# Optimization experiments

Hardware: AMD Instinct MI355X
Metric: run time of the kernel (lower is better)

The kernel has to match this reference:

```python
import jax, jax.numpy as jnp
import numpy as np
from jax import lax

HEAD_DIM = 32
SCALE = HEAD_DIM ** -0.5
BN_EPS = 1e-5


def _bn_relu(x, g, b):
    # training-mode BatchNorm2d over (B,H,W) per channel, biased variance, then ReLU
    mean = jnp.mean(x, axis=(0, 1, 2))
    var = jnp.var(x, axis=(0, 1, 2))
    y = (x - mean) * lax.rsqrt(var + BN_EPS) * g + b
    return jax.nn.relu(y)


def _pool2x2(y, op):
    # AvgPool2d/MaxPool2d(kernel=2, stride=2) on [B,pH,pW,C]
    B, pH, pW, C = y.shape
    y = y.reshape(B, pH // 2, 2, pW // 2, 2, C)
    return op(y, axis=(2, 4))


def setup_inputs() -> dict:
    key = jax.random.key(0)
    ks = jax.random.split(key, 12)
    B, H, W, C, pC = 16, 32, 32, 512, 256
    s = lambda k, shape, fan: jax.random.normal(k, shape, jnp.float32) * (fan ** -0.5)
    return {
        "x": jax.random.normal(ks[0], (B, H, W, C), jnp.float32),
        "prevx": jax.random.normal(ks[1], (B, 2 * H, 2 * W, pC), jnp.float32),
        "w_prev_qkv": s(ks[2], (C, pC), pC),          # Linear(prev_dim->dim), no bias
        "w_qkv": s(ks[3], (C, C), C),                  # Linear(dim->dim), no bias
        "fuse_w": s(ks[4], (2 * C, C), 2 * C),         # 1x1 conv as [Cin, Cout]
        "fuse_b": jax.random.normal(ks[5], (C,), jnp.float32) * 0.01,
        "bn1_g": jnp.ones((C,), jnp.float32) + jax.random.normal(ks[6], (C,), jnp.float32) * 0.01,
        "bn1_b": jax.random.normal(ks[7], (C,), jnp.float32) * 0.01,
        "out_w": s(ks[8], (3, 3, C, C), 9 * C),        # 3x3 conv HWIO
        "out_b": jax.random.normal(ks[9], (C,), jnp.float32) * 0.01,
        "bn2_g": jnp.ones((C,), jnp.float32) + jax.random.normal(ks[10], (C,), jnp.float32) * 0.01,
        "bn2_b": jax.random.normal(ks[11], (C,), jnp.float32) * 0.01,
        "gamma": jnp.array([0.3], jnp.float32),
        "beta": jnp.array([0.4], jnp.float32),
    }


def reference(x, prevx, w_prev_qkv, w_qkv, fuse_w, fuse_b, bn1_g, bn1_b,
              out_w, out_b, bn2_g, bn2_b, gamma, beta):
    B, H, W, C = x.shape
    N = H * W

    prevqkv = prevx @ w_prev_qkv.T                       # [B,2H,2W,C]
    qkv = (x @ w_qkv.T).reshape(B, N, C)                 # [B,N,C]
    avg_kv = _pool2x2(prevqkv, jnp.mean).reshape(B, -1, C)
    max_kv = _pool2x2(prevqkv, jnp.max).reshape(B, -1, C)

    def attn(q, k, v):
        a = jax.nn.softmax(jnp.einsum('bnc,bmc->bnm', q, k) * SCALE, axis=-1)
        o = jnp.einsum('bnm,bmc->bnc', a, v)
        # faithful to torch: (attn@v).transpose(1,2).reshape(B,H,W,-1)
        return jnp.swapaxes(o, 1, 2).reshape(B, H, W, C)

    x_now = attn(qkv, qkv, qkv)
    avgx_prev = attn(qkv, avg_kv, avg_kv)
    maxx_prev = attn(qkv, max_kv, max_kv)
    x_prev = beta[0] * avgx_prev + (1.0 - beta[0]) * maxx_prev

    cat = jnp.concatenate([x_now, x_prev], axis=-1)      # [B,H,W,2C]
    fusx = _bn_relu(jnp.einsum('bhwi,io->bhwo', cat, fuse_w) + fuse_b, bn1_g, bn1_b)
    x = x + gamma[0] * fusx

    y = lax.conv_general_dilated(x, out_w, window_strides=(1, 1), padding='SAME',
                                 dimension_numbers=('NHWC', 'HWIO', 'NHWC')) + out_b
    return _bn_relu(y, bn2_g, bn2_b)
```

## Files before the change

kernel.cpp:

```cpp
#include <hip/hip_runtime.h>
#include <hip/hip_bf16.h>

#define B_   16
#define C_   512
#define N_   1024
#define NTOK 16384
#define SCALE_ 0.17677669529663687f
#define EPS_ 1e-5f

typedef __attribute__((ext_vector_type(8))) short bf16x8;
typedef __attribute__((ext_vector_type(4))) float f32x4;
typedef __attribute__((ext_vector_type(4))) short sh4;

#define GLOBAL_AS __attribute__((address_space(1)))
#define LDS_AS    __attribute__((address_space(3)))
#define MFMA16 __builtin_amdgcn_mfma_f32_16x16x32_bf16

__device__ __forceinline__ short f2bs(float v){
    __hip_bfloat16 h = __float2bfloat16(v);
    return *reinterpret_cast<short*>(&h);
}
__device__ __forceinline__ float bs2f(short s){
    __hip_bfloat16 h = *reinterpret_cast<__hip_bfloat16*>(&s);
    return __bfloat162float(h);
}
__device__ __forceinline__ void gload16(const void* g, void* l){
    __builtin_amdgcn_global_load_lds((const GLOBAL_AS unsigned int*)g,
                                     (LDS_AS unsigned int*)l, 16, 0, 0);
}

enum { AG_ROW = 0, AG_POOL = 1, AG_FUSE = 2, AG_CONV = 3, AG_SEL3 = 4 };
enum { EP_QKV = 0, EP_POOL = 1, EP_BIAS_F32 = 5, EP_SPLIT_F32 = 6, EP_PVN = 7 };
enum { ORD_INNER_N = 0, ORD_INNER_M = 1 };

__global__ __launch_bounds__(256) void k_zero(float* p, int n){
    int i = blockIdx.x*256 + threadIdx.x;
    if (i < n) p[i] = 0.f;
}

__global__ __launch_bounds__(256) void k_cast(const float* __restrict__ s, short* __restrict__ d, int n){
    int i = (blockIdx.x*256 + threadIdx.x)*4;
    if (i >= n) return;
    float4 v = *reinterpret_cast<const float4*>(s + i);
    sh4 o; o[0]=f2bs(v.x); o[1]=f2bs(v.y); o[2]=f2bs(v.z); o[3]=f2bs(v.w);
    *reinterpret_cast<sh4*>(d + i) = o;
}

__global__ __launch_bounds__(256) void k_tcast(const float* __restrict__ src, short* __restrict__ dst,
                                               int R, int Cc){
    __shared__ float t[32][33];
    int bx = blockIdx.x*32, by = blockIdx.y*32;
    int tx = threadIdx.x & 31, ty = threadIdx.x >> 5;
    #pragma unroll
    for (int i = 0; i < 32; i += 8)
        t[ty+i][tx] = src[(size_t)(by+ty+i)*Cc + bx+tx];
    __syncthreads();
    #pragma unroll
    for (int i = 0; i < 32; i += 8)
        dst[(size_t)(bx+ty+i)*R + by+tx] = f2bs(t[tx][ty+i]);
}

template<int AM, int EP, int ORDER, int NX, int NY, int NZ, int NT, int KT, int KROW, int KSPLIT,
         long ASTR, long BSTR>
__global__ __launch_bounds__(256) void k_mm(const short* __restrict__ A,
                                            const short* __restrict__ Bt,
                                            const short* __restrict__ A2,
                                            const float* __restrict__ sc0,
                                            void* __restrict__ O0,
                                            void* __restrict__ O1,
                                            void* __restrict__ O2,
                                            void* __restrict__ O3){
    __shared__ short Asm[128*32];
    __shared__ short Bsm[128*32];
    const int tid = threadIdx.x, wave = tid >> 6, lane = tid & 63;

    constexpr int nwg = NX*NY*NZ;
    constexpr int q8 = nwg >> 3, r8 = nwg & 7;
    int orig = blockIdx.x;
    int xcd = orig & 7, idx8 = orig >> 3;
    int wg = (xcd < r8 ? xcd*(q8+1) : r8*(q8+1) + (xcd - r8)*q8) + idx8;
    int bz = wg / (NX*NY);
    int rem = wg - bz*(NX*NY);
    int nx, my;
    if constexpr (ORDER == ORD_INNER_N){ my = rem / NX; nx = rem - my*NX; }
    else                               { nx = rem / NY; my = rem - nx*NY; }

    const int m0 = my*128, n0 = nx*128;
    const short* Ab;
    if constexpr (AM == AG_SEL3){
        const short* base = (bz < 16) ? A : (bz < 32) ? A2 : (const short*)O3;
        Ab = base + (size_t)(bz & 15)*ASTR;
    } else {
        Ab = A + (size_t)bz*ASTR;
    }
    const short* Bb = Bt + (size_t)bz*BSTR;

    f32x4 acc[4][4];
    #pragma unroll
    for (int i = 0; i < 4; ++i)
        #pragma unroll
        for (int j = 0; j < 4; ++j)
            acc[i][j] = (f32x4){0.f,0.f,0.f,0.f};

    const int wm = (wave >> 1)*64, wn = (wave & 1)*64;
    const int lrow = lane & 15, lk = (lane >> 4)*8;

    for (int k0 = 0; k0 < KT; k0 += 32){
        #pragma unroll
        for (int is = 0; is < 2; ++is){
            int fl = is*256 + tid;
            int r = fl >> 2, ccol = (fl & 3)*8;
            int kk = bz*KSPLIT + k0 + ccol;
            const short* ga;
            if constexpr (AM == AG_ROW || AM == AG_SEL3){
                ga = Ab + (size_t)(m0 + r)*KROW + kk;
            } else if constexpr (AM == AG_POOL){
                int m = m0 + r;
                int b = m >> 12, rem2 = m & 4095, g = rem2 >> 2, qd = rem2 & 3;
                int srow = (b*64 + (g>>5)*2 + (qd>>1))*64 + (g&31)*2 + (qd&1);
                ga = Ab + (size_t)srow*KROW + kk;
            } else if constexpr (AM == AG_FUSE){
                int m = m0 + r;
                int b = m >> 10, rem2 = m & 1023, h = rem2 >> 5, w = rem2 & 31;
                const short* src = (kk < 512) ? A : A2;
                ga = src + ((size_t)(b*512 + h*16 + (w>>1))*1024 + ((w&1)<<9) + (kk & 511));
            } else {
                int m = m0 + r;
                int b = m >> 10, rem2 = m & 1023, h = rem2 >> 5, w = rem2 & 31;
                int tap = kk >> 9, ic = kk & 511;
                int dh = tap/3 - 1, dw = tap - (tap/3)*3 - 1;
                int hs = h + dh, wd = w + dw;
                if (hs >= 0 && hs < 32 && wd >= 0 && wd < 32)
                    ga = A + ((size_t)((b*32 + hs)*32 + wd)*512 + ic);
                else
                    ga = A2;
            }
            gload16(ga, &Asm[(is*4 + wave)*512]);
            const short* gb = Bb + (size_t)(n0 + r)*KROW + kk;
            gload16(gb, &Bsm[(is*4 + wave)*512]);
        }
        __syncthreads();
        bf16x8 af[4], bfr[4];
        #pragma unroll
        for (int mi = 0; mi < 4; ++mi)
            af[mi] = *(const bf16x8*)&Asm[(wm + mi*16 + lrow)*32 + lk];
        #pragma unroll
        for (int nj = 0; nj < 4; ++nj)
            bfr[nj] = *(const bf16x8*)&Bsm[(wn + nj*16 + lrow)*32 + lk];
        #pragma unroll
        for (int mi = 0; mi < 4; ++mi)
            #pragma unroll
            for (int nj = 0; nj < 4; ++nj)
                acc[mi][nj] = MFMA16(af[mi], bfr[nj], acc[mi][nj], 0, 0, 0);
        __syncthreads();
    }

    const int lg = lane >> 4;
    #pragma unroll
    for (int mi = 0; mi < 4; ++mi)
        #pragma unroll
        for (int nj = 0; nj < 4; ++nj){
            int c  = n0 + wn + nj*16 + lrow;
            int r0 = m0 + wm + mi*16 + lg*4;
            f32x4 v = acc[mi][nj];
            if constexpr (EP == EP_QKV){
                sh4 t4;
                #pragma unroll
                for (int rg = 0; rg < 4; ++rg){
                    short s = f2bs(v[rg]);
                    ((short*)O0)[(size_t)(r0+rg)*NT + c] = s;
                    t4[rg] = s;
                }
                int b = r0 >> 10, t = r0 & 1023;
                *reinterpret_cast<sh4*>((short*)O1 + ((size_t)(b*512 + c))*1024 + t) = t4;
            } else if constexpr (EP == EP_POOL){
                float av = 0.25f*(v[0]+v[1]+v[2]+v[3]);
                float mx = fmaxf(fmaxf(v[0],v[1]), fmaxf(v[2],v[3]));
                int g = r0 >> 2;
                int b = g >> 10, t = g & 1023;
                ((short*)O0)[(size_t)g*512 + c] = f2bs(av);
                ((short*)O2)[(size_t)g*512 + c] = f2bs(mx);
                ((short*)O1)[((size_t)(b*512 + c))*1024 + t] = f2bs(av);
                ((short*)O3)[((size_t)(b*512 + c))*1024 + t] = f2bs(mx);
            } else if constexpr (EP == EP_PVN){
                short* Ob = ((bz < 16) ? (short*)O0 : (bz < 32) ? (short*)O1 : (short*)O2)
                            + (size_t)(bz & 15)*524288;
                float sc = sc0[(size_t)bz*1024 + c];
                #pragma unroll
                for (int rg = 0; rg < 4; ++rg)
                    Ob[(size_t)(r0+rg)*NT + c] = f2bs(v[rg]*sc);
            } else if constexpr (EP == EP_SPLIT_F32){
                float* O = (float*)O0 + (size_t)bz*((long)NTOK*NT);
                #pragma unroll
                for (int rg = 0; rg < 4; ++rg)
                    O[(size_t)(r0+rg)*NT + c] = v[rg];
            } else {
                float bias = sc0[c];
                #pragma unroll
                for (int rg = 0; rg < 4; ++rg)
                    ((float*)O0)[(size_t)(r0+rg)*NT + c] = v[rg] + bias;
            }
        }
}

__global__ __launch_bounds__(256) void k_scorep(
    const short* __restrict__ Q,
    const short* __restrict__ K0, const short* __restrict__ K1, const short* __restrict__ K2,
    short* __restrict__ P, float* __restrict__ linvp)
{
    __shared__ short Kls[32*512];
    __shared__ short Pls[4][16][40];

    const int tid = threadIdx.x, wave = tid >> 6, lane = tid & 63;
    const int lrow = lane & 15, hi = lane >> 4;

    int orig = blockIdx.x;
    int wg = (orig & 7)*96 + (orig >> 3);
    int a = wg >> 8, rem = wg & 255;
    int b = rem >> 4, qt = rem & 15;

    const short* Kb = (a == 0 ? K0 : a == 1 ? K1 : K2) + (size_t)b*524288;
    const short* Qb = Q + (size_t)b*524288;
    short* Pb = P + ((size_t)(a*16 + b) << 20);
    const int m0 = qt*64 + wave*16;

    bf16x8 q[16];
    #pragma unroll
    for (int ks = 0; ks < 16; ++ks)
        q[ks] = *(const bf16x8*)&Qb[(size_t)(m0 + lrow)*512 + ks*32 + hi*8];

    const int swk = (lrow & 7) << 4;
    float lsum[4] = {0.f,0.f,0.f,0.f};

    for (int kv = 0; kv < 1024; kv += 32){
        #pragma unroll
        for (int it = 0; it < 8; ++it){
            int r = it*4 + wave;
            gload16(Kb + (size_t)(kv + r)*512 + (size_t)((lane ^ (r & 7))*8), &Kls[r*512]);
        }
        __syncthreads();
        f32x4 s0 = {0.f,0.f,0.f,0.f}, s1 = {0.f,0.f,0.f,0.f};
        #pragma unroll
        for (int ks = 0; ks < 16; ++ks){
            bf16x8 b0 = *(const bf16x8*)&Kls[lrow*512      + (((ks*64 + hi*16) ^ swk) >> 1)];
            bf16x8 b1 = *(const bf16x8*)&Kls[(16+lrow)*512 + (((ks*64 + hi*16) ^ swk) >> 1)];
            s0 = MFMA16(q[ks], b0, s0, 0, 0, 0);
            s1 = MFMA16(q[ks], b1, s1, 0, 0, 0);
        }
        #pragma unroll
        for (int r = 0; r < 4; ++r){
            float p0 = __expf(fminf(s0[r]*SCALE_, 80.f));
            float p1 = __expf(fminf(s1[r]*SCALE_, 80.f));
            lsum[r] += p0 + p1;
            Pls[wave][hi*4 + r][lrow]      = f2bs(p0);
            Pls[wave][hi*4 + r][16 + lrow] = f2bs(p1);
        }
        bf16x8 pk = *(const bf16x8*)&Pls[wave][lane >> 2][(lane & 3)*8];
        *reinterpret_cast<bf16x8*>(&Pb[(size_t)(m0 + (lane >> 2))*1024 + kv + (lane & 3)*8]) = pk;
        __syncthreads();
    }

    #pragma unroll
    for (int r = 0; r < 4; ++r){
        float s = lsum[r];
        #pragma unroll
        for (int off = 1; off < 16; off <<= 1) s += __shfl_xor(s, off);
        if (lrow == 0)
            linvp[(size_t)(a*16 + b)*1024 + m0 + hi*4 + r] = 1.f/s;
    }
}

__global__ __launch_bounds__(256) void k_combine(const short* __restrict__ av,
                                                 const short* __restrict__ mx,
                                                 short* __restrict__ o,
                                                 const float* __restrict__ beta){
    int i = (blockIdx.x*256 + threadIdx.x)*8;
    float be = beta[0];
    bf16x8 va = *(const bf16x8*)&av[i];
    bf16x8 vm = *(const bf16x8*)&mx[i];
    bf16x8 vo;
    #pragma unroll
    for (int j = 0; j < 8; ++j)
        vo[j] = f2bs(be*bs2f(va[j]) + (1.f - be)*bs2f(vm[j]));
    *reinterpret_cast<bf16x8*>(&o[i]) = vo;
}

__global__ __launch_bounds__(256) void k_stats(const float* __restrict__ in,
                                               float* __restrict__ sum, float* __restrict__ sumsq){
    int t = threadIdx.x, c0 = t*2, r0 = blockIdx.x*32;
    float s0=0, s1=0, q0=0, q1=0;
    for (int r = 0; r < 32; ++r){
        float2 v = *reinterpret_cast<const float2*>(in + (size_t)(r0+r)*C_ + c0);
        s0 += v.x; q0 += v.x*v.x; s1 += v.y; q1 += v.y*v.y;
    }
    atomicAdd(&sum[c0],   s0); atomicAdd(&sum[c0+1],   s1);
    atomicAdd(&sumsq[c0], q0); atomicAdd(&sumsq[c0+1], q1);
}

__global__ __launch_bounds__(256) void k_stats2(const float* __restrict__ p0,
                                                const float* __restrict__ p1,
                                                const float* __restrict__ bias,
                                                float* __restrict__ Y,
                                                float* __restrict__ sum, float* __restrict__ sumsq){
    int t = threadIdx.x, c0 = t*2, r0 = blockIdx.x*32;
    float b0 = bias[c0], b1 = bias[c0+1];
    float s0=0, s1=0, q0=0, q1=0;
    for (int r = 0; r < 32; ++r){
        size_t off = (size_t)(r0+r)*C_ + c0;
        float2 a = *reinterpret_cast<const float2*>(p0 + off);
        float2 b = *reinterpret_cast<const float2*>(p1 + off);
        float v0 = a.x + b.x + b0, v1 = a.y + b.y + b1;
        float2 ov; ov.x = v0; ov.y = v1;
        *reinterpret_cast<float2*>(Y + off) = ov;
        s0 += v0; q0 += v0*v0; s1 += v1; q1 += v1*v1;
    }
    atomicAdd(&sum[c0],   s0); atomicAdd(&sum[c0+1],   s1);
    atomicAdd(&sumsq[c0], q0); atomicAdd(&sumsq[c0+1], q1);
}

__global__ __launch_bounds__(256) void k_apply1(const float* __restrict__ fusx,
                                                const float* __restrict__ x,
                                                const float* __restrict__ sum,
                                                const float* __restrict__ sumsq,
                                                const float* __restrict__ g,
                                                const float* __restrict__ bb,
                                                const float* __restrict__ gamma,
                                                short* __restrict__ x2q){
    int idx = blockIdx.x*256 + threadIdx.x;
    int c = idx & (C_-1);
    float mean = sum[c]*(1.f/NTOK);
    float var  = sumsq[c]*(1.f/NTOK) - mean*mean;
    float t = (fusx[idx] - mean)*rsqrtf(var + EPS_)*g[c] + bb[c];
    x2q[idx] = f2bs(x[idx] + gamma[0]*fmaxf(t, 0.f));
}

__global__ __launch_bounds__(256) void k_apply2(float* __restrict__ Y,
                                                const float* __restrict__ sum,
                                                const float* __restrict__ sumsq,
                                                const float* __restrict__ g,
                                                const float* __restrict__ bb){
    int idx = blockIdx.x*256 + threadIdx.x;
    int c = idx & (C_-1);
    float mean = sum[c]*(1.f/NTOK);
    float var  = sumsq[c]*(1.f/NTOK) - mean*mean;
    float t = (Y[idx] - mean)*rsqrtf(var + EPS_)*g[c] + bb[c];
    Y[idx] = fmaxf(t, 0.f);
}

extern "C" void kernel_launch(void* const* d_in, const int* in_sizes, int n_in,
                              void* d_out, int out_size, void* d_ws, size_t ws_size,
                              hipStream_t stream){
    const float* x      = (const float*)d_in[0];
    const float* prevx  = (const float*)d_in[1];
    const float* w_prev = (const float*)d_in[2];
    const float* w_qkv  = (const float*)d_in[3];
    const float* fuse_w = (const float*)d_in[4];
    const float* fuse_b = (const float*)d_in[5];
    const float* bn1_g  = (const float*)d_in[6];
    const float* bn1_b  = (const float*)d_in[7];
    const float* out_w  = (const float*)d_in[8];
    const float* out_b  = (const float*)d_in[9];
    const float* bn2_g  = (const float*)d_in[10];
    const float* bn2_b  = (const float*)d_in[11];
    const float* gamma  = (const float*)d_in[12];
    const float* beta   = (const float*)d_in[13];
    float* out = (float*)d_out;

    char* ws8 = (char*)d_ws;
    short* pxq  = (short*)(ws8 + 0);
    short* xq   = (short*)(ws8 + 33554432);
    short* Pall = (short*)(ws8 + 0);
    float* cpart= (float*)(ws8 + 0);
    short* qkvT = (short*)(ws8 + 100663296);
    short* x2q  = (short*)(ws8 + 100663296);
    short* avgkT= (short*)(ws8 + 117440512);
    short* maxkT= (short*)(ws8 + 134217728);
    short* prevT= maxkT;
    short* nowT = (short*)(ws8 + 150994944);
    short* avgk = nowT;
    short* avgT = (short*)(ws8 + 167772160);
    short* maxk = avgT;
    short* maxT = (short*)(ws8 + 184549376);
    float* fusx = (float*)(ws8 + 184549376);
    short* qkv  = (short*)(ws8 + 201326592);
    short* wqT  = (short*)(ws8 + 218103808);
    short* wpT  = (short*)(ws8 + 218628096);
    short* wfT  = (short*)(ws8 + 218890240);
    short* wcT  = (short*)(ws8 + 219938816);
    float* st   = (float*)(ws8 + 224657408);
    short* zpg  = (short*)(ws8 + 224665600);
    float* linv = (float*)(ws8 + 224666624);
    float *s1sum = st, *s1sq = st + 512, *s2sum = st + 1024, *s2sq = st + 1536;

    dim3 blk(256);
    k_zero<<<9, blk, 0, stream>>>(st, 2304);
    k_cast<<<8192, blk, 0, stream>>>(x, xq, 8388608);
    k_cast<<<256,  blk, 0, stream>>>(w_qkv, wqT, 262144);
    k_cast<<<128,  blk, 0, stream>>>(w_prev, wpT, 131072);
    k_tcast<<<dim3(16, 32),  blk, 0, stream>>>(fuse_w, wfT, 1024, 512);
    k_tcast<<<dim3(16, 144), blk, 0, stream>>>(out_w, wcT, 4608, 512);
    k_cast<<<16384, blk, 0, stream>>>(prevx, pxq, 16777216);

    k_mm<AG_ROW, EP_QKV, ORD_INNER_N, 4, 128, 1, 512, 512, 512, 0, 0L, 0L>
        <<<512, blk, 0, stream>>>(xq, wqT, nullptr, nullptr,
                                  qkv, qkvT, nullptr, nullptr);
    k_mm<AG_POOL, EP_POOL, ORD_INNER_N, 4, 512, 1, 512, 256, 256, 0, 0L, 0L>
        <<<2048, blk, 0, stream>>>(pxq, wpT, nullptr, nullptr,
                                   avgk, avgkT, maxk, maxkT);
    k_scorep<<<768, blk, 0, stream>>>(qkv, qkv, avgk, maxk, Pall, linv);
    k_mm<AG_SEL3, EP_PVN, ORD_INNER_M, 8, 4, 48, 1024, 1024, 1024, 0, 524288L, 1048576L>
        <<<1536, blk, 0, stream>>>(qkvT, Pall, avgkT, linv,
                                   nowT, avgT, maxT, maxkT);
    k_combine<<<4096, blk, 0, stream>>>(avgT, maxT, prevT, beta);
    k_mm<AG_FUSE, EP_BIAS_F32, ORD_INNER_N, 4, 128, 1, 512, 1024, 1024, 0, 0L, 0L>
        <<<512, blk, 0, stream>>>(nowT, wfT, prevT, fuse_b,
                                  fusx, nullptr, nullptr, nullptr);
    k_stats<<<512, blk, 0, stream>>>(fusx, s1sum, s1sq);
    k_apply1<<<32768, blk, 0, stream>>>(fusx, x, s1sum, s1sq, bn1_g, bn1_b, gamma, x2q);
    k_mm<AG_CONV, EP_SPLIT_F32, ORD_INNER_N, 4, 128, 2, 512, 2304, 4608, 2304, 0L, 0L>
        <<<1024, blk, 0, stream>>>(x2q, wcT, zpg, nullptr,
                                   cpart, nullptr, nullptr, nullptr);
    k_stats2<<<512, blk, 0, stream>>>(cpart, cpart + (size_t)NTOK*C_, out_b, out, s2sum, s2sq);
    k_apply2<<<32768, blk, 0, stream>>>(out, s2sum, s2sq, bn2_g, bn2_b);
}
```

Baseline: 518.3 us.

## Fuse BN1 statistics into fuse GEMM epilogue and store intermediates as bf16

```diff
diff --git a/kernel.cpp b/kernel.cpp
--- a/kernel.cpp
+++ b/kernel.cpp
@@ -30,7 +30,7 @@
 }
 
 enum { AG_ROW = 0, AG_POOL = 1, AG_FUSE = 2, AG_CONV = 3, AG_SEL3 = 4 };
-enum { EP_QKV = 0, EP_POOL = 1, EP_BIAS_F32 = 5, EP_SPLIT_F32 = 6, EP_PVN = 7 };
+enum { EP_QKV = 0, EP_POOL = 1, EP_PVN = 7, EP_FUSE_STATS = 8, EP_SPLIT_BF16 = 9 };
 enum { ORD_INNER_N = 0, ORD_INNER_M = 1 };
 
 __global__ __launch_bounds__(256) void k_zero(float* p, int n){
@@ -156,6 +156,41 @@
     }
 
     const int lg = lane >> 4;
+
+    if constexpr (EP == EP_FUSE_STATS){
+        float* redS = (float*)Asm;
+        float* redQ = (float*)Bsm;
+        #pragma unroll
+        for (int nj = 0; nj < 4; ++nj){
+            int c = n0 + wn + nj*16 + lrow;
+            float bias = sc0[c];
+            float s = 0.f, qq = 0.f;
+            #pragma unroll
+            for (int mi = 0; mi < 4; ++mi){
+                int r0 = m0 + wm + mi*16 + lg*4;
+                #pragma unroll
+                for (int rg = 0; rg < 4; ++rg){
+                    float val = acc[mi][nj][rg] + bias;
+                    s += val; qq += val*val;
+                    ((short*)O0)[(size_t)(r0+rg)*NT + c] = f2bs(val);
+                }
+            }
+            int chl = wn + nj*16 + lrow;
+            int slot = (wave >> 1)*4 + lg;
+            redS[chl*8 + slot] = s;
+            redQ[chl*8 + slot] = qq;
+        }
+        __syncthreads();
+        if (tid < 128){
+            float S = 0.f, Q = 0.f;
+            #pragma unroll
+            for (int k = 0; k < 8; ++k){ S += redS[tid*8 + k]; Q += redQ[tid*8 + k]; }
+            atomicAdd(&((float*)O1)[n0 + tid], S);
+            atomicAdd(&((float*)O2)[n0 + tid], Q);
+        }
+        return;
+    }
+
     #pragma unroll
     for (int mi = 0; mi < 4; ++mi)
         #pragma unroll
@@ -189,16 +224,11 @@
                 #pragma unroll
                 for (int rg = 0; rg < 4; ++rg)
                     Ob[(size_t)(r0+rg)*NT + c] = f2bs(v[rg]*sc);
-            } else if constexpr (EP == EP_SPLIT_F32){
-                float* O = (float*)O0 + (size_t)bz*((long)NTOK*NT);
+            } else {
+                short* O = (short*)O0 + (size_t)bz*((long)NTOK*NT);
                 #pragma unroll
                 for (int rg = 0; rg < 4; ++rg)
-                    O[(size_t)(r0+rg)*NT + c] = v[rg];
-            } else {
-                float bias = sc0[c];
-                #pragma unroll
-                for (int rg = 0; rg < 4; ++rg)
-                    ((float*)O0)[(size_t)(r0+rg)*NT + c] = v[rg] + bias;
+                    O[(size_t)(r0+rg)*NT + c] = f2bs(v[rg]);
             }
         }
 }
@@ -285,20 +315,8 @@
     *reinterpret_cast<bf16x8*>(&o[i]) = vo;
 }
 
-__global__ __launch_bounds__(256) void k_stats(const float* __restrict__ in,
-                                               float* __restrict__ sum, float* __restrict__ sumsq){
-    int t = threadIdx.x, c0 = t*2, r0 = blockIdx.x*32;
-    float s0=0, s1=0, q0=0, q1=0;
-    for (int r = 0; r < 32; ++r){
-        float2 v = *reinterpret_cast<const float2*>(in + (size_t)(r0+r)*C_ + c0);
-        s0 += v.x; q0 += v.x*v.x; s1 += v.y; q1 += v.y*v.y;
-    }
-    atomicAdd(&sum[c0],   s0); atomicAdd(&sum[c0+1],   s1);
-    atomicAdd(&sumsq[c0], q0); atomicAdd(&sumsq[c0+1], q1);
-}
-
-__global__ __launch_bounds__(256) void k_stats2(const float* __restrict__ p0,
-                                                const float* __restrict__ p1,
+__global__ __launch_bounds__(256) void k_stats2(const short* __restrict__ p0,
+                                                const short* __restrict__ p1,
                                                 const float* __restrict__ bias,
                                                 float* __restrict__ Y,
                                                 float* __restrict__ sum, float* __restrict__ sumsq){
@@ -307,9 +325,10 @@
     float s0=0, s1=0, q0=0, q1=0;
     for (int r = 0; r < 32; ++r){
         size_t off = (size_t)(r0+r)*C_ + c0;
-        float2 a = *reinterpret_cast<const float2*>(p0 + off);
-        float2 b = *reinterpret_cast<const float2*>(p1 + off);
-        float v0 = a.x + b.x + b0, v1 = a.y + b.y + b1;
+        unsigned a = *reinterpret_cast<const unsigned*>(p0 + off);
+        unsigned b = *reinterpret_cast<const unsigned*>(p1 + off);
+        float v0 = bs2f((short)(a & 0xffff)) + bs2f((short)(b & 0xffff)) + b0;
+        float v1 = bs2f((short)(a >> 16))    + bs2f((short)(b >> 16))    + b1;
         float2 ov; ov.x = v0; ov.y = v1;
         *reinterpret_cast<float2*>(Y + off) = ov;
         s0 += v0; q0 += v0*v0; s1 += v1; q1 += v1*v1;
@@ -318,7 +337,7 @@
     atomicAdd(&sumsq[c0], q0); atomicAdd(&sumsq[c0+1], q1);
 }
 
-__global__ __launch_bounds__(256) void k_apply1(const float* __restrict__ fusx,
+__global__ __launch_bounds__(256) void k_apply1(const short* __restrict__ fusxq,
                                                 const float* __restrict__ x,
                                                 const float* __restrict__ sum,
                                                 const float* __restrict__ sumsq,
@@ -326,12 +345,22 @@
                                                 const float* __restrict__ bb,
                                                 const float* __restrict__ gamma,
                                                 short* __restrict__ x2q){
-    int idx = blockIdx.x*256 + threadIdx.x;
-    int c = idx & (C_-1);
-    float mean = sum[c]*(1.f/NTOK);
-    float var  = sumsq[c]*(1.f/NTOK) - mean*mean;
-    float t = (fusx[idx] - mean)*rsqrtf(var + EPS_)*g[c] + bb[c];
-    x2q[idx] = f2bs(x[idx] + gamma[0]*fmaxf(t, 0.f));
+    int i4 = (blockIdx.x*256 + threadIdx.x)*4;
+    int c = i4 & (C_-1);
+    sh4 f = *reinterpret_cast<const sh4*>(fusxq + i4);
+    float4 xv = *reinterpret_cast<const float4*>(x + i4);
+    float gm = gamma[0];
+    sh4 o;
+    #pragma unroll
+    for (int j = 0; j < 4; ++j){
+        int cj = c + j;
+        float mean = sum[cj]*(1.f/NTOK);
+        float var  = sumsq[cj]*(1.f/NTOK) - mean*mean;
+        float t = (bs2f(f[j]) - mean)*rsqrtf(var + EPS_)*g[cj] + bb[cj];
+        float xj = (j==0) ? xv.x : (j==1) ? xv.y : (j==2) ? xv.z : xv.w;
+        o[j] = f2bs(xj + gm*fmaxf(t, 0.f));
+    }
+    *reinterpret_cast<sh4*>(x2q + i4) = o;
 }
 
 __global__ __launch_bounds__(256) void k_apply2(float* __restrict__ Y,
@@ -339,12 +368,20 @@
                                                 const float* __restrict__ sumsq,
                                                 const float* __restrict__ g,
                                                 const float* __restrict__ bb){
-    int idx = blockIdx.x*256 + threadIdx.x;
-    int c = idx & (C_-1);
-    float mean = sum[c]*(1.f/NTOK);
-    float var  = sumsq[c]*(1.f/NTOK) - mean*mean;
-    float t = (Y[idx] - mean)*rsqrtf(var + EPS_)*g[c] + bb[c];
-    Y[idx] = fmaxf(t, 0.f);
+    int i4 = (blockIdx.x*256 + threadIdx.x)*4;
+    int c = i4 & (C_-1);
+    float4 v = *reinterpret_cast<float4*>(Y + i4);
+    float o[4] = {v.x, v.y, v.z, v.w};
+    #pragma unroll
+    for (int j = 0; j < 4; ++j){
+        int cj = c + j;
+        float mean = sum[cj]*(1.f/NTOK);
+        float var  = sumsq[cj]*(1.f/NTOK) - mean*mean;
+        float t = (o[j] - mean)*rsqrtf(var + EPS_)*g[cj] + bb[cj];
+        o[j] = fmaxf(t, 0.f);
+    }
+    float4 ov; ov.x = o[0]; ov.y = o[1]; ov.z = o[2]; ov.w = o[3];
+    *reinterpret_cast<float4*>(Y + i4) = ov;
 }
 
 extern "C" void kernel_launch(void* const* d_in, const int* in_sizes, int n_in,
@@ -370,7 +407,7 @@
     short* pxq  = (short*)(ws8 + 0);
     short* xq   = (short*)(ws8 + 33554432);
     short* Pall = (short*)(ws8 + 0);
-    float* cpart= (float*)(ws8 + 0);
+    short* cpartq = (short*)(ws8 + 0);
     short* qkvT = (short*)(ws8 + 100663296);
     short* x2q  = (short*)(ws8 + 100663296);
     short* avgkT= (short*)(ws8 + 117440512);
@@ -381,7 +418,7 @@
     short* avgT = (short*)(ws8 + 167772160);
     short* maxk = avgT;
     short* maxT = (short*)(ws8 + 184549376);
-    float* fusx = (float*)(ws8 + 184549376);
+    short* fusxq= (short*)(ws8 + 184549376);
     short* qkv  = (short*)(ws8 + 201326592);
     short* wqT  = (short*)(ws8 + 218103808);
     short* wpT  = (short*)(ws8 + 218628096);
@@ -412,14 +449,13 @@
         <<<1536, blk, 0, stream>>>(qkvT, Pall, avgkT, linv,
                                    nowT, avgT, maxT, maxkT);
     k_combine<<<4096, blk, 0, stream>>>(avgT, maxT, prevT, beta);
-    k_mm<AG_FUSE, EP_BIAS_F32, ORD_INNER_N, 4, 128, 1, 512, 1024, 1024, 0, 0L, 0L>
+    k_mm<AG_FUSE, EP_FUSE_STATS, ORD_INNER_N, 4, 128, 1, 512, 1024, 1024, 0, 0L, 0L>
         <<<512, blk, 0, stream>>>(nowT, wfT, prevT, fuse_b,
-                                  fusx, nullptr, nullptr, nullptr);
-    k_stats<<<512, blk, 0, stream>>>(fusx, s1sum, s1sq);
-    k_apply1<<<32768, blk, 0, stream>>>(fusx, x, s1sum, s1sq, bn1_g, bn1_b, gamma, x2q);
-    k_mm<AG_CONV, EP_SPLIT_F32, ORD_INNER_N, 4, 128, 2, 512, 2304, 4608, 2304, 0L, 0L>
+                                  fusxq, s1sum, s1sq, nullptr);
+    k_apply1<<<8192, blk, 0, stream>>>(fusxq, x, s1sum, s1sq, bn1_g, bn1_b, gamma, x2q);
+    k_mm<AG_CONV, EP_SPLIT_BF16, ORD_INNER_N, 4, 128, 2, 512, 2304, 4608, 2304, 0L, 0L>
         <<<1024, blk, 0, stream>>>(x2q, wcT, zpg, nullptr,
-                                   cpart, nullptr, nullptr, nullptr);
-    k_stats2<<<512, blk, 0, stream>>>(cpart, cpart + (size_t)NTOK*C_, out_b, out, s2sum, s2sq);
-    k_apply2<<<32768, blk, 0, stream>>>(out, s2sum, s2sq, bn2_g, bn2_b);
-}
+                                   cpartq, nullptr, nullptr, nullptr);
+    k_stats2<<<512, blk, 0, stream>>>(cpartq, cpartq + (size_t)NTOK*C_, out_b, out, s2sum, s2sq);
+    k_apply2<<<8192, blk, 0, stream>>>(out, s2sum, s2sq, bn2_g, bn2_b);
+}
```

Measured after the change: 490.5 us. 5.4% less time.
